# Kernel optimization log

Measured on AMD Instinct MI355X. Metric: run time of the kernel, lower is better.

Reference implementation:

```python
import jax, jax.numpy as jnp
import numpy as np

K = 1024        # knowledge_num == feature dim == number of knowledge nodes
E_N = 30000     # exercise_num
E_DIR = 65536
E_UND = 65536
E_EK = 120000


def _uniform(k, shape, scale):
    return jax.random.uniform(k, shape, jnp.float32, -scale, scale)


def setup_inputs() -> dict:
    key = jax.random.key(0)
    ks = jax.random.split(key, 20)
    s = 1.0 / np.sqrt(K)        # nn.Linear default init bound
    s2 = 1.0 / np.sqrt(2 * K)
    return {
        'exer_emb': jax.random.normal(ks[0], (E_N, K), jnp.float32),
        'kn_emb': jax.random.normal(ks[1], (K, K), jnp.float32),
        'dir_src': jax.random.randint(ks[2], (E_DIR,), 0, K),
        'dir_dst': jax.random.randint(ks[3], (E_DIR,), 0, K),
        'und_src': jax.random.randint(ks[4], (E_UND,), 0, K),
        'und_dst': jax.random.randint(ks[5], (E_UND,), 0, K),
        # e_from_k: src are knowledge nodes offset into combined [exer; kn] graph
        'ek_src': jax.random.randint(ks[6], (E_EK,), 0, K) + E_N,
        'ek_dst': jax.random.randint(ks[7], (E_EK,), 0, E_N),
        'W_dir': _uniform(ks[8], (K, K), s),
        'a_dir': _uniform(ks[9], (2 * K,), s2),
        'W_und': _uniform(ks[10], (K, K), s),
        'a_und': _uniform(ks[11], (2 * K,), s2),
        'W_ek': _uniform(ks[12], (K, K), s),
        'a_ek': _uniform(ks[13], (2 * K,), s2),
        'k_w1': _uniform(ks[14], (2 * K,), s2), 'k_b1': _uniform(ks[15], (), s2),
        'k_w2': _uniform(ks[16], (2 * K,), s2), 'k_b2': _uniform(ks[17], (), s2),
        'e_w1': _uniform(ks[18], (2 * K,), s2), 'e_b1': _uniform(ks[19], (), s2),
    }


def gat_layer(h, W, a, src, dst, num_nodes):
    """GraphLayer: z = h@W; e_ij = a^T [z_src, z_dst]; softmax over in-edges; h_i = sum alpha*z_src."""
    z = h @ W                                   # [N, D]
    d = z.shape[1]
    e = (z @ a[:d])[src] + (z @ a[d:])[dst]     # [E] edge logits (split avoids [E,2D] concat)
    m = jax.ops.segment_max(e, dst, num_segments=num_nodes)
    ex = jnp.exp(e - m[dst])
    den = jax.ops.segment_sum(ex, dst, num_segments=num_nodes)
    alpha = ex / den[dst]                       # per-dst softmax (mailbox softmax)
    return jax.ops.segment_sum(alpha[:, None] * z[src], dst, num_segments=num_nodes)


def reference(exer_emb, kn_emb, dir_src, dir_dst, und_src, und_dst, ek_src, ek_dst,
              W_dir, a_dir, W_und, a_und, W_ek, a_ek,
              k_w1, k_b1, k_w2, k_b2, e_w1, e_b1):
    k_directed = gat_layer(kn_emb, W_dir, a_dir, dir_src, dir_dst, K)
    k_undirected = gat_layer(kn_emb, W_und, a_und, und_src, und_dst, K)
    e_k = jnp.concatenate([exer_emb, kn_emb], axis=0)           # [E_N+K, K]
    e_from_k = gat_layer(e_k, W_ek, a_ek, ek_src, ek_dst, E_N + K)

    # knowledge gating: softmax over two concat-linear scores
    A, B, C = kn_emb, k_directed, k_undirected
    s1 = A @ k_w1[:K] + B @ k_w1[K:] + k_b1                     # [K]
    s2 = A @ k_w2[:K] + C @ k_w2[K:] + k_b2
    sc = jax.nn.softmax(jnp.stack([s1, s2], axis=1), axis=1)    # [K, 2]
    kn_out = A + sc[:, 0:1] * B + sc[:, 1:2] * C

    # exercise gating: raw linear score (no softmax)
    Be = e_from_k[:E_N]
    se = exer_emb @ e_w1[:K] + Be @ e_w1[K:] + e_b1             # [E_N]
    exer_out = exer_emb + se[:, None] * Be
    return (exer_out, kn_out)
```

## Files before the change

kernel.cpp:

```cpp
#include <hip/hip_runtime.h>

#define E_N 30000
#define KDIM 1024
#define E_DIRN 65536
#define E_UNDN 65536
#define E_EKN 120000
#define NB (1024 + 1024 + E_N)
#define TOT_E (E_DIRN + E_UNDN + E_EKN)
#define ZERON (3 * KDIM + NB)
#define CAPK 192
#define CAPE 48
#define EKBASE (2048 * CAPK)
#define NEDGE_SLOTS (EKBASE + E_N * CAPE)

typedef __attribute__((ext_vector_type(8))) short bfrag8;
typedef __attribute__((ext_vector_type(4))) float facc4;
typedef __attribute__((ext_vector_type(4))) float f4v;

static __device__ __forceinline__ unsigned short f2bf(float f) {
    unsigned int u = __float_as_uint(f);
    u += 0x7fffu + ((u >> 16) & 1u);
    return (unsigned short)(u >> 16);
}
static __device__ __forceinline__ unsigned int pack2(float lo, float hi) {
    return (unsigned int)f2bf(lo) | ((unsigned int)f2bf(hi) << 16);
}
static __device__ __forceinline__ float bf2f(short u) {
    return __uint_as_float(((unsigned int)(unsigned short)u) << 16);
}
static __device__ __forceinline__ float dot4(f4v a, f4v b) {
    return a.x * b.x + a.y * b.y + a.z * b.z + a.w * b.w;
}
static __device__ __forceinline__ void gload16(const void* g, void* l) {
    __builtin_amdgcn_global_load_lds(
        (const __attribute__((address_space(1))) unsigned int*)g,
        (__attribute__((address_space(3))) unsigned int*)l, 16, 0, 0);
}

__global__ __launch_bounds__(256) void prep(
    const float* __restrict__ kn, const float* __restrict__ W0,
    const float* __restrict__ W1, const float* __restrict__ W2,
    unsigned short* __restrict__ knb, unsigned short* __restrict__ Wtall,
    int* __restrict__ zero_base)
{
    int z = blockIdx.z;
    int tx = threadIdx.x, ty = threadIdx.y;
    if (z == 4) {
        int idx = (blockIdx.y * 32 + blockIdx.x) * 256 + ty * 32 + tx;
        if (idx < ZERON) zero_base[idx] = 0;
        return;
    }
    if (z == 3) {
        int b = blockIdx.y * 32 + blockIdx.x;
        int t = ty * 32 + tx;
        int idx = b * 1024 + t * 4;
        float4 a = *(const float4*)&kn[idx];
        uint2 o; o.x = pack2(a.x, a.y); o.y = pack2(a.z, a.w);
        *(uint2*)&knb[idx] = o;
        return;
    }
    const float* W = (z == 0) ? W0 : (z == 1) ? W1 : W2;
    unsigned short* Wt = Wtall + (size_t)z * KDIM * KDIM;
    __shared__ float tile[32][33];
    int nb = blockIdx.x * 32, kb = blockIdx.y * 32;
#pragma unroll
    for (int r0 = 0; r0 < 32; r0 += 8)
        tile[r0 + ty][tx] = W[(size_t)(kb + r0 + ty) * KDIM + nb + tx];
    __syncthreads();
#pragma unroll
    for (int r0 = 0; r0 < 32; r0 += 8)
        Wt[(size_t)(nb + r0 + ty) * KDIM + kb + tx] = f2bf(tile[tx][r0 + ty]);
}

__global__ __launch_bounds__(256) void gemm_mfma(
    const unsigned short* __restrict__ Ab,
    const unsigned short* __restrict__ Btall,
    const float* __restrict__ a_dir, const float* __restrict__ a_und,
    const float* __restrict__ a_ek,
    unsigned short* __restrict__ Zb, float* __restrict__ zdot)
{
    int z = blockIdx.z;
    const unsigned short* Bb = Btall + (size_t)z * KDIM * KDIM;
    unsigned short* C = Zb + (size_t)z * KDIM * KDIM;
    const float* avec = (z == 0) ? a_dir : (z == 1) ? a_und : a_ek;
    __shared__ alignas(16) unsigned short As[2][64 * 64];
    __shared__ alignas(16) unsigned short Bs[2][64 * 64];
    int tid = threadIdx.x;
    int lane = tid & 63, wv = tid >> 6;
    int wr = wv >> 1, wc = wv & 1;
    int tm = blockIdx.x * 64, tn = blockIdx.y * 64;
    int srow = lane >> 3, sch = lane & 7;
    facc4 acc[2][2] = {};

    auto stage = [&](int buf, int kk) {
#pragma unroll
        for (int t = 0; t < 2; ++t) {
            int r0 = wv * 16 + t * 8;
            int row = r0 + srow;
            gload16(&Ab[(size_t)(tm + row) * KDIM + kk + ((sch ^ (row & 7)) << 3)],
                    &As[buf][r0 * 64]);
        }
#pragma unroll
        for (int t = 0; t < 2; ++t) {
            int r0 = wv * 16 + t * 8;
            int row = r0 + srow;
            gload16(&Bb[(size_t)(tn + row) * KDIM + kk + ((sch ^ (row & 7)) << 3)],
                    &Bs[buf][r0 * 64]);
        }
    };
    auto compute = [&](int buf) {
#pragma unroll
        for (int ks = 0; ks < 2; ++ks) {
            bfrag8 af[2], bfr[2];
            int kch = ks * 4 + (lane >> 4);
#pragma unroll
            for (int f = 0; f < 2; ++f) {
                int ar = wr * 32 + f * 16 + (lane & 15);
                af[f] = *(const bfrag8*)&As[buf][ar * 64 + ((kch ^ (ar & 7)) << 3)];
                int bcol = wc * 32 + f * 16 + (lane & 15);
                bfr[f] = *(const bfrag8*)&Bs[buf][bcol * 64 + ((kch ^ (bcol & 7)) << 3)];
            }
#pragma unroll
            for (int i = 0; i < 2; ++i)
#pragma unroll
                for (int j = 0; j < 2; ++j)
                    acc[i][j] = __builtin_amdgcn_mfma_f32_16x16x32_bf16(af[i], bfr[j], acc[i][j], 0, 0, 0);
        }
    };

    stage(0, 0);
    __syncthreads();
    int cur = 0;
    for (int kk = 64; kk < KDIM; kk += 64) {
        stage(cur ^ 1, kk);
        compute(cur);
        __syncthreads();
        cur ^= 1;
    }
    compute(cur);

    int col0 = lane & 15, r0 = (lane >> 4) * 4;
    float av2[2];
#pragma unroll
    for (int j = 0; j < 2; ++j) av2[j] = avec[tn + wc * 32 + j * 16 + col0];
#pragma unroll
    for (int i = 0; i < 2; ++i)
#pragma unroll
        for (int j = 0; j < 2; ++j) {
            int row = tm + wr * 32 + i * 16 + r0;
            int col = tn + wc * 32 + j * 16 + col0;
#pragma unroll
            for (int r = 0; r < 4; ++r)
                C[(size_t)(row + r) * KDIM + col] = f2bf(acc[i][j][r]);
        }
#pragma unroll
    for (int i = 0; i < 2; ++i)
#pragma unroll
        for (int r = 0; r < 4; ++r) {
            float t = acc[i][0][r] * av2[0] + acc[i][1][r] * av2[1];
            t += __shfl_xor(t, 1); t += __shfl_xor(t, 2);
            t += __shfl_xor(t, 4); t += __shfl_xor(t, 8);
            if ((lane & 15) == 0)
                atomicAdd(&zdot[z * KDIM + tm + wr * 32 + i * 16 + r0 + r], t);
        }
}

__global__ __launch_bounds__(256) void scatter_edges(
    const int* __restrict__ dir_src, const int* __restrict__ dir_dst,
    const int* __restrict__ und_src, const int* __restrict__ und_dst,
    const int* __restrict__ ek_src, const int* __restrict__ ek_dst,
    const float* __restrict__ zdot, int* __restrict__ counts,
    int2* __restrict__ edge_sw)
{
    int i = blockIdx.x * 256 + threadIdx.x;
    int bin, s; float w;
    if (i < E_DIRN) { bin = dir_dst[i]; s = dir_src[i]; w = expf(zdot[s]); }
    else if (i < E_DIRN + E_UNDN) {
        int loc = i - E_DIRN; bin = 1024 + und_dst[loc]; s = und_src[loc]; w = expf(zdot[1024 + s]);
    } else if (i < TOT_E) {
        int loc = i - E_DIRN - E_UNDN; bin = 2048 + ek_dst[loc]; s = ek_src[loc] - E_N; w = expf(zdot[2048 + s]);
    } else return;
    int slot = atomicAdd(&counts[bin], 1);
    if (bin < 2048) {
        if (slot < CAPK) edge_sw[(size_t)bin * CAPK + slot] = make_int2(s, __float_as_int(w));
    } else {
        if (slot < CAPE) edge_sw[EKBASE + (size_t)(bin - 2048) * CAPE + slot] = make_int2(s, __float_as_int(w));
    }
}

__global__ __launch_bounds__(256) void gather_all(
    const unsigned short* __restrict__ Zb, const int2* __restrict__ edge_sw,
    const int* __restrict__ counts,
    const float* __restrict__ exer, const float* __restrict__ kn,
    const float* __restrict__ k_w1, const float* __restrict__ k_b1,
    const float* __restrict__ k_w2, const float* __restrict__ k_b2,
    const float* __restrict__ e_w1, const float* __restrict__ e_b1,
    float* __restrict__ out)
{
    __shared__ float bcs[2][KDIM];
    __shared__ float parts[4];
    int tid = threadIdx.x;
    if (blockIdx.x < KDIM) {
        int row = blockIdx.x;
        int wv = tid >> 6, lane = tid & 63;
        int g = wv >> 1, half = wv & 1;
        int bin = (g << 10) + row;
        int n = min(counts[bin], CAPK);
        size_t start = (size_t)bin * CAPK;
        const bfrag8* Zp = (const bfrag8*)(Zb + (size_t)g * KDIM * KDIM) + half * 64 + lane;
        float b8[8] = {};
        float den = 0.f;
        for (int c0 = 0; c0 < n; c0 += 64) {
            int m = min(64, n - c0);
            int s = 0; float w = 0.f;
            if (lane < m) {
                int2 ew = edge_sw[start + c0 + lane];
                s = ew.x; w = __int_as_float(ew.y);
            }
            int j = 0;
            for (; j + 4 <= m; j += 4) {
                int   s0 = __shfl(s, j), s1 = __shfl(s, j+1), s2 = __shfl(s, j+2), s3 = __shfl(s, j+3);
                float w0 = __shfl(w, j), w1 = __shfl(w, j+1), w2 = __shfl(w, j+2), w3 = __shfl(w, j+3);
                bfrag8 v0 = Zp[(size_t)s0 * 128], v1 = Zp[(size_t)s1 * 128];
                bfrag8 v2 = Zp[(size_t)s2 * 128], v3 = Zp[(size_t)s3 * 128];
#pragma unroll
                for (int k = 0; k < 8; ++k)
                    b8[k] += w0*bf2f(v0[k]) + w1*bf2f(v1[k]) + w2*bf2f(v2[k]) + w3*bf2f(v3[k]);
                den += w0 + w1 + w2 + w3;
            }
            for (; j + 2 <= m; j += 2) {
                int   s0 = __shfl(s, j), s1 = __shfl(s, j+1);
                float w0 = __shfl(w, j), w1 = __shfl(w, j+1);
                bfrag8 v0 = Zp[(size_t)s0 * 128], v1 = Zp[(size_t)s1 * 128];
#pragma unroll
                for (int k = 0; k < 8; ++k) b8[k] += w0*bf2f(v0[k]) + w1*bf2f(v1[k]);
                den += w0 + w1;
            }
            if (j < m) {
                int   s0 = __shfl(s, j);
                float w0 = __shfl(w, j);
                bfrag8 v0 = Zp[(size_t)s0 * 128];
#pragma unroll
                for (int k = 0; k < 8; ++k) b8[k] += w0*bf2f(v0[k]);
                den += w0;
            }
        }
        float inv = (n > 0) ? 1.f / den : 0.f;
#pragma unroll
        for (int k = 0; k < 8; ++k) b8[k] *= inv;
        const float* wvp = g ? k_w2 : k_w1;
        int cb = half * 512 + lane * 8;
        f4v A0 = *(const f4v*)&kn[(size_t)row * KDIM + cb];
        f4v A1 = *(const f4v*)&kn[(size_t)row * KDIM + cb + 4];
        f4v wa0 = *(const f4v*)&wvp[cb];
        f4v wa1 = *(const f4v*)&wvp[cb + 4];
        f4v wb0 = *(const f4v*)&wvp[KDIM + cb];
        f4v wb1 = *(const f4v*)&wvp[KDIM + cb + 4];
        f4v bb0 = {b8[0], b8[1], b8[2], b8[3]};
        f4v bb1 = {b8[4], b8[5], b8[6], b8[7]};
        float p = dot4(A0, wa0) + dot4(A1, wa1) + dot4(bb0, wb0) + dot4(bb1, wb1);
#pragma unroll
        for (int off = 32; off > 0; off >>= 1) p += __shfl_xor(p, off);
        if (lane == 0) parts[wv] = p;
        *(f4v*)&bcs[g][cb] = bb0;
        *(f4v*)&bcs[g][cb + 4] = bb1;
        __syncthreads();
        float s1 = parts[0] + parts[1] + k_b1[0];
        float s2 = parts[2] + parts[3] + k_b2[0];
        float mx = fmaxf(s1, s2);
        float e1 = expf(s1 - mx), e2 = expf(s2 - mx);
        float isum = 1.f / (e1 + e2);
        float sc0 = e1 * isum, sc1 = e2 * isum;
        int col = tid * 4;
        f4v A = *(const f4v*)&kn[(size_t)row * KDIM + col];
        f4v B = *(const f4v*)&bcs[0][col];
        f4v Cc = *(const f4v*)&bcs[1][col];
        *(f4v*)&out[(size_t)(E_N + row) * KDIM + col] = A + sc0 * B + sc1 * Cc;
        return;
    }
    int row = ((blockIdx.x - KDIM) * 256 + tid) >> 6;
    int lane = tid & 63;
    int n = min(counts[2048 + row], CAPE);
    size_t start = EKBASE + (size_t)row * CAPE;
    const f4v* xr = (const f4v*)&exer[(size_t)row * KDIM];
    f4v x00 = xr[2 * lane];
    f4v x01 = xr[2 * lane + 1];
    f4v x10 = xr[2 * lane + 128];
    f4v x11 = xr[2 * lane + 129];
    const bfrag8* Zp = (const bfrag8*)(Zb + (size_t)2 * KDIM * KDIM);
    float b0[8] = {}, b1[8] = {};
    float den = 0.f;
    {
        int s = 0; float w = 0.f;
        if (lane < n) {
            int2 ew = edge_sw[start + lane];
            s = ew.x; w = __int_as_float(ew.y);
        }
        int j = 0;
        for (; j + 4 <= n; j += 4) {
            int   s0 = __shfl(s, j), s1 = __shfl(s, j+1), s2 = __shfl(s, j+2), s3 = __shfl(s, j+3);
            float w0 = __shfl(w, j), w1 = __shfl(w, j+1), w2 = __shfl(w, j+2), w3 = __shfl(w, j+3);
            const bfrag8* z0 = Zp + (size_t)s0 * 128;
            const bfrag8* z1 = Zp + (size_t)s1 * 128;
            const bfrag8* z2 = Zp + (size_t)s2 * 128;
            const bfrag8* z3 = Zp + (size_t)s3 * 128;
            bfrag8 a0 = z0[lane], a1 = z0[lane + 64];
            bfrag8 c0v = z1[lane], c1 = z1[lane + 64];
            bfrag8 d0 = z2[lane], d1 = z2[lane + 64];
            bfrag8 e0 = z3[lane], e1 = z3[lane + 64];
#pragma unroll
            for (int k = 0; k < 8; ++k) {
                b0[k] += w0*bf2f(a0[k]) + w1*bf2f(c0v[k]) + w2*bf2f(d0[k]) + w3*bf2f(e0[k]);
                b1[k] += w0*bf2f(a1[k]) + w1*bf2f(c1[k]) + w2*bf2f(d1[k]) + w3*bf2f(e1[k]);
            }
            den += w0 + w1 + w2 + w3;
        }
        for (; j + 2 <= n; j += 2) {
            int   s0 = __shfl(s, j), s1 = __shfl(s, j+1);
            float w0 = __shfl(w, j), w1 = __shfl(w, j+1);
            const bfrag8* z0 = Zp + (size_t)s0 * 128;
            const bfrag8* z1 = Zp + (size_t)s1 * 128;
            bfrag8 a0 = z0[lane], a1 = z0[lane + 64];
            bfrag8 c0v = z1[lane], c1 = z1[lane + 64];
#pragma unroll
            for (int k = 0; k < 8; ++k) {
                b0[k] += w0*bf2f(a0[k]) + w1*bf2f(c0v[k]);
                b1[k] += w0*bf2f(a1[k]) + w1*bf2f(c1[k]);
            }
            den += w0 + w1;
        }
        if (j < n) {
            int   s0 = __shfl(s, j);
            float w0 = __shfl(w, j);
            const bfrag8* z0 = Zp + (size_t)s0 * 128;
            bfrag8 a0 = z0[lane], a1 = z0[lane + 64];
#pragma unroll
            for (int k = 0; k < 8; ++k) {
                b0[k] += w0*bf2f(a0[k]);
                b1[k] += w0*bf2f(a1[k]);
            }
            den += w0;
        }
    }
    float inv = (n > 0) ? 1.f / den : 0.f;
#pragma unroll
    for (int k = 0; k < 8; ++k) { b0[k] *= inv; b1[k] *= inv; }
    const f4v* wap = (const f4v*)e_w1;
    const f4v* wbp = (const f4v*)(e_w1 + KDIM);
    f4v wa0 = wap[2*lane], wa1 = wap[2*lane+1], wa2 = wap[2*lane+128], wa3 = wap[2*lane+129];
    f4v wb0 = wbp[2*lane], wb1 = wbp[2*lane+1], wb2 = wbp[2*lane+128], wb3 = wbp[2*lane+129];
    f4v bb0 = {b0[0], b0[1], b0[2], b0[3]};
    f4v bb1 = {b0[4], b0[5], b0[6], b0[7]};
    f4v bb2 = {b1[0], b1[1], b1[2], b1[3]};
    f4v bb3 = {b1[4], b1[5], b1[6], b1[7]};
    float p = dot4(x00, wa0) + dot4(x01, wa1) + dot4(x10, wa2) + dot4(x11, wa3)
            + dot4(bb0, wb0) + dot4(bb1, wb1) + dot4(bb2, wb2) + dot4(bb3, wb3);
#pragma unroll
    for (int off = 32; off > 0; off >>= 1) p += __shfl_xor(p, off);
    float se = p + e_b1[0];
    f4v* op = (f4v*)&out[(size_t)row * KDIM];
    op[2 * lane]       = x00 + se * bb0;
    op[2 * lane + 1]   = x01 + se * bb1;
    op[2 * lane + 128] = x10 + se * bb2;
    op[2 * lane + 129] = x11 + se * bb3;
}

extern "C" void kernel_launch(void* const* d_in, const int* in_sizes, int n_in,
                              void* d_out, int out_size, void* d_ws, size_t ws_size,
                              hipStream_t stream)
{
    (void)in_sizes; (void)n_in; (void)out_size; (void)ws_size;
    const float* exer  = (const float*)d_in[0];
    const float* kn    = (const float*)d_in[1];
    const int* dir_src = (const int*)d_in[2];
    const int* dir_dst = (const int*)d_in[3];
    const int* und_src = (const int*)d_in[4];
    const int* und_dst = (const int*)d_in[5];
    const int* ek_src  = (const int*)d_in[6];
    const int* ek_dst  = (const int*)d_in[7];
    const float* W_dir = (const float*)d_in[8];
    const float* a_dir = (const float*)d_in[9];
    const float* W_und = (const float*)d_in[10];
    const float* a_und = (const float*)d_in[11];
    const float* W_ek  = (const float*)d_in[12];
    const float* a_ek  = (const float*)d_in[13];
    const float* k_w1  = (const float*)d_in[14];
    const float* k_b1  = (const float*)d_in[15];
    const float* k_w2  = (const float*)d_in[16];
    const float* k_b2  = (const float*)d_in[17];
    const float* e_w1  = (const float*)d_in[18];
    const float* e_b1  = (const float*)d_in[19];

    char* ws = (char*)d_ws;
    unsigned short* Zb = (unsigned short*)ws; ws += (size_t)3 * KDIM * KDIM * 2;
    float* zdot    = (float*)ws; ws += 3 * KDIM * 4;
    int* counts    = (int*)ws;   ws += NB * 4;
    int2* edge_sw  = (int2*)ws;  ws += (size_t)NEDGE_SLOTS * 8;
    unsigned short* knb = (unsigned short*)ws; ws += (size_t)KDIM * KDIM * 2;
    unsigned short* Wtb = (unsigned short*)ws; ws += (size_t)3 * KDIM * KDIM * 2;

    prep<<<dim3(32, 32, 5), dim3(32, 8), 0, stream>>>(kn, W_dir, W_und, W_ek,
                                                      knb, Wtb, (int*)zdot);
    gemm_mfma<<<dim3(16, 16, 3), 256, 0, stream>>>(knb, Wtb, a_dir, a_und, a_ek,
                                                   Zb, zdot);
    int eb = (TOT_E + 255) / 256;
    scatter_edges<<<eb, 256, 0, stream>>>(dir_src, dir_dst, und_src, und_dst,
                                          ek_src, ek_dst, zdot, counts, edge_sw);

    float* out = (float*)d_out;
    gather_all<<<KDIM + 7500, 256, 0, stream>>>(Zb, edge_sw, counts,
                                                exer, kn, k_w1, k_b1, k_w2, k_b2,
                                                e_w1, e_b1, out);
}
```

Before: 130.8 us.

## Make exercise gather persistent with prefetch of next row's edges, shrink CAPE

The exercise part of gather_all becomes a grid-stride persistent loop over 1024 blocks of 4 waves. Each wave prefetches the next row's edge list and count while it processes the current row. The e_w1 weights are loaded once per wave rather than once per row, and the per-row edge capacity is cut from 48 to 32, which shrinks the edge slot buffer. With ek in-degree averaging about 4, the smaller cap is safe for these inputs, but any row with more than 32 edges would be silently truncated, and there are fewer waves in flight to hide latency.

```diff
diff --git a/kernel.cpp b/kernel.cpp
--- a/kernel.cpp
+++ b/kernel.cpp
@@ -9,9 +9,10 @@
 #define TOT_E (E_DIRN + E_UNDN + E_EKN)
 #define ZERON (3 * KDIM + NB)
 #define CAPK 192
-#define CAPE 48
+#define CAPE 32
 #define EKBASE (2048 * CAPK)
 #define NEDGE_SLOTS (EKBASE + E_N * CAPE)
+#define EXBLK 1024
 
 typedef __attribute__((ext_vector_type(8))) short bfrag8;
 typedef __attribute__((ext_vector_type(4))) float facc4;
@@ -278,91 +279,106 @@
         *(f4v*)&out[(size_t)(E_N + row) * KDIM + col] = A + sc0 * B + sc1 * Cc;
         return;
     }
-    int row = ((blockIdx.x - KDIM) * 256 + tid) >> 6;
+    const int NW = EXBLK * 4;
+    int wid = (blockIdx.x - KDIM) * 4 + (tid >> 6);
     int lane = tid & 63;
-    int n = min(counts[2048 + row], CAPE);
-    size_t start = EKBASE + (size_t)row * CAPE;
-    const f4v* xr = (const f4v*)&exer[(size_t)row * KDIM];
-    f4v x00 = xr[2 * lane];
-    f4v x01 = xr[2 * lane + 1];
-    f4v x10 = xr[2 * lane + 128];
-    f4v x11 = xr[2 * lane + 129];
     const bfrag8* Zp = (const bfrag8*)(Zb + (size_t)2 * KDIM * KDIM);
-    float b0[8] = {}, b1[8] = {};
-    float den = 0.f;
-    {
-        int s = 0; float w = 0.f;
-        if (lane < n) {
-            int2 ew = edge_sw[start + lane];
-            s = ew.x; w = __int_as_float(ew.y);
-        }
-        int j = 0;
-        for (; j + 4 <= n; j += 4) {
-            int   s0 = __shfl(s, j), s1 = __shfl(s, j+1), s2 = __shfl(s, j+2), s3 = __shfl(s, j+3);
-            float w0 = __shfl(w, j), w1 = __shfl(w, j+1), w2 = __shfl(w, j+2), w3 = __shfl(w, j+3);
-            const bfrag8* z0 = Zp + (size_t)s0 * 128;
-            const bfrag8* z1 = Zp + (size_t)s1 * 128;
-            const bfrag8* z2 = Zp + (size_t)s2 * 128;
-            const bfrag8* z3 = Zp + (size_t)s3 * 128;
-            bfrag8 a0 = z0[lane], a1 = z0[lane + 64];
-            bfrag8 c0v = z1[lane], c1 = z1[lane + 64];
-            bfrag8 d0 = z2[lane], d1 = z2[lane + 64];
-            bfrag8 e0 = z3[lane], e1 = z3[lane + 64];
-#pragma unroll
-            for (int k = 0; k < 8; ++k) {
-                b0[k] += w0*bf2f(a0[k]) + w1*bf2f(c0v[k]) + w2*bf2f(d0[k]) + w3*bf2f(e0[k]);
-                b1[k] += w0*bf2f(a1[k]) + w1*bf2f(c1[k]) + w2*bf2f(d1[k]) + w3*bf2f(e1[k]);
-            }
-            den += w0 + w1 + w2 + w3;
-        }
-        for (; j + 2 <= n; j += 2) {
-            int   s0 = __shfl(s, j), s1 = __shfl(s, j+1);
-            float w0 = __shfl(w, j), w1 = __shfl(w, j+1);
-            const bfrag8* z0 = Zp + (size_t)s0 * 128;
-            const bfrag8* z1 = Zp + (size_t)s1 * 128;
-            bfrag8 a0 = z0[lane], a1 = z0[lane + 64];
-            bfrag8 c0v = z1[lane], c1 = z1[lane + 64];
-#pragma unroll
-            for (int k = 0; k < 8; ++k) {
-                b0[k] += w0*bf2f(a0[k]) + w1*bf2f(c0v[k]);
-                b1[k] += w0*bf2f(a1[k]) + w1*bf2f(c1[k]);
-            }
-            den += w0 + w1;
-        }
-        if (j < n) {
-            int   s0 = __shfl(s, j);
-            float w0 = __shfl(w, j);
-            const bfrag8* z0 = Zp + (size_t)s0 * 128;
-            bfrag8 a0 = z0[lane], a1 = z0[lane + 64];
-#pragma unroll
-            for (int k = 0; k < 8; ++k) {
-                b0[k] += w0*bf2f(a0[k]);
-                b1[k] += w0*bf2f(a1[k]);
-            }
-            den += w0;
-        }
-    }
-    float inv = (n > 0) ? 1.f / den : 0.f;
-#pragma unroll
-    for (int k = 0; k < 8; ++k) { b0[k] *= inv; b1[k] *= inv; }
     const f4v* wap = (const f4v*)e_w1;
     const f4v* wbp = (const f4v*)(e_w1 + KDIM);
     f4v wa0 = wap[2*lane], wa1 = wap[2*lane+1], wa2 = wap[2*lane+128], wa3 = wap[2*lane+129];
     f4v wb0 = wbp[2*lane], wb1 = wbp[2*lane+1], wb2 = wbp[2*lane+128], wb3 = wbp[2*lane+129];
-    f4v bb0 = {b0[0], b0[1], b0[2], b0[3]};
-    f4v bb1 = {b0[4], b0[5], b0[6], b0[7]};
-    f4v bb2 = {b1[0], b1[1], b1[2], b1[3]};
-    f4v bb3 = {b1[4], b1[5], b1[6], b1[7]};
-    float p = dot4(x00, wa0) + dot4(x01, wa1) + dot4(x10, wa2) + dot4(x11, wa3)
-            + dot4(bb0, wb0) + dot4(bb1, wb1) + dot4(bb2, wb2) + dot4(bb3, wb3);
-#pragma unroll
-    for (int off = 32; off > 0; off >>= 1) p += __shfl_xor(p, off);
-    float se = p + e_b1[0];
-    f4v* op = (f4v*)&out[(size_t)row * KDIM];
-    op[2 * lane]       = x00 + se * bb0;
-    op[2 * lane + 1]   = x01 + se * bb1;
-    op[2 * lane + 128] = x10 + se * bb2;
-    op[2 * lane + 129] = x11 + se * bb3;
+    float eb1 = e_b1[0];
+
+    int row = wid;
+    int2 e_cur = make_int2(0, 0);
+    int n_cur = 0;
+    if (lane < CAPE) e_cur = edge_sw[EKBASE + (size_t)row * CAPE + lane];
+    n_cur = counts[2048 + row];
+    while (row < E_N) {
+        int nrow = row + NW;
+        int2 e_nxt = make_int2(0, 0);
+        int n_nxt = 0;
+        if (nrow < E_N) {
+            if (lane < CAPE) e_nxt = edge_sw[EKBASE + (size_t)nrow * CAPE + lane];
+            n_nxt = counts[2048 + nrow];
+        }
+        const f4v* xr = (const f4v*)&exer[(size_t)row * KDIM];
+        f4v x00 = xr[2 * lane];
+        f4v x01 = xr[2 * lane + 1];
+        f4v x10 = xr[2 * lane + 128];
+        f4v x11 = xr[2 * lane + 129];
+        int n = min(n_cur, CAPE);
+        float b0[8] = {}, b1[8] = {};
+        float den = 0.f;
+        {
+            int s = e_cur.x; float w = __int_as_float(e_cur.y);
+            int j = 0;
+            for (; j + 4 <= n; j += 4) {
+                int   s0 = __shfl(s, j), s1 = __shfl(s, j+1), s2 = __shfl(s, j+2), s3 = __shfl(s, j+3);
+                float w0 = __shfl(w, j), w1 = __shfl(w, j+1), w2 = __shfl(w, j+2), w3 = __shfl(w, j+3);
+                const bfrag8* z0 = Zp + (size_t)s0 * 128;
+                const bfrag8* z1 = Zp + (size_t)s1 * 128;
+                const bfrag8* z2 = Zp + (size_t)s2 * 128;
+                const bfrag8* z3 = Zp + (size_t)s3 * 128;
+                bfrag8 a0 = z0[lane], a1 = z0[lane + 64];
+                bfrag8 c0v = z1[lane], c1 = z1[lane + 64];
+                bfrag8 d0 = z2[lane], d1 = z2[lane + 64];
+                bfrag8 e0 = z3[lane], e1 = z3[lane + 64];
+#pragma unroll
+                for (int k = 0; k < 8; ++k) {
+                    b0[k] += w0*bf2f(a0[k]) + w1*bf2f(c0v[k]) + w2*bf2f(d0[k]) + w3*bf2f(e0[k]);
+                    b1[k] += w0*bf2f(a1[k]) + w1*bf2f(c1[k]) + w2*bf2f(d1[k]) + w3*bf2f(e1[k]);
+                }
+                den += w0 + w1 + w2 + w3;
+            }
+            for (; j + 2 <= n; j += 2) {
+                int   s0 = __shfl(s, j), s1 = __shfl(s, j+1);
+                float w0 = __shfl(w, j), w1 = __shfl(w, j+1);
+                const bfrag8* z0 = Zp + (size_t)s0 * 128;
+                const bfrag8* z1 = Zp + (size_t)s1 * 128;
+                bfrag8 a0 = z0[lane], a1 = z0[lane + 64];
+                bfrag8 c0v = z1[lane], c1 = z1[lane + 64];
+#pragma unroll
+                for (int k = 0; k < 8; ++k) {
+                    b0[k] += w0*bf2f(a0[k]) + w1*bf2f(c0v[k]);
+                    b1[k] += w0*bf2f(a1[k]) + w1*bf2f(c1[k]);
+                }
+                den += w0 + w1;
+            }
+            if (j < n) {
+                int   s0 = __shfl(s, j);
+                float w0 = __shfl(w, j);
+                const bfrag8* z0 = Zp + (size_t)s0 * 128;
+                bfrag8 a0 = z0[lane], a1 = z0[lane + 64];
+#pragma unroll
+                for (int k = 0; k < 8; ++k) {
+                    b0[k] += w0*bf2f(a0[k]);
+                    b1[k] += w0*bf2f(a1[k]);
+                }
+                den += w0;
+            }
+        }
+        float inv = (n > 0) ? 1.f / den : 0.f;
+#pragma unroll
+        for (int k = 0; k < 8; ++k) { b0[k] *= inv; b1[k] *= inv; }
+        f4v bb0 = {b0[0], b0[1], b0[2], b0[3]};
+        f4v bb1 = {b0[4], b0[5], b0[6], b0[7]};
+        f4v bb2 = {b1[0], b1[1], b1[2], b1[3]};
+        f4v bb3 = {b1[4], b1[5], b1[6], b1[7]};
+        float p = dot4(x00, wa0) + dot4(x01, wa1) + dot4(x10, wa2) + dot4(x11, wa3)
+                + dot4(bb0, wb0) + dot4(bb1, wb1) + dot4(bb2, wb2) + dot4(bb3, wb3);
+#pragma unroll
+        for (int off = 32; off > 0; off >>= 1) p += __shfl_xor(p, off);
+        float se = p + eb1;
+        f4v* op = (f4v*)&out[(size_t)row * KDIM];
+        op[2 * lane]       = x00 + se * bb0;
+        op[2 * lane + 1]   = x01 + se * bb1;
+        op[2 * lane + 128] = x10 + se * bb2;
+        op[2 * lane + 129] = x11 + se * bb3;
+        row = nrow;
+        e_cur = e_nxt;
+        n_cur = n_nxt;
+    }
 }
 
 extern "C" void kernel_launch(void* const* d_in, const int* in_sizes, int n_in,
@@ -408,7 +424,7 @@
                                           ek_src, ek_dst, zdot, counts, edge_sw);
 
     float* out = (float*)d_out;
-    gather_all<<<KDIM + 7500, 256, 0, stream>>>(Zb, edge_sw, counts,
-                                                exer, kn, k_w1, k_b1, k_w2, k_b2,
-                                                e_w1, e_b1, out);
-}
+    gather_all<<<KDIM + EXBLK, 256, 0, stream>>>(Zb, edge_sw, counts,
+                                                 exer, kn, k_w1, k_b1, k_w2, k_b2,
+                                                 e_w1, e_b1, out);
+}
```

After: 146.2 us. +11.7%, slower.
